# Performance work log

Measured on AMD Instinct MI355X. Metric: run time of the kernel, lower is better.

Reference implementation:

```python
import jax, jax.numpy as jnp
import numpy as np
import math

B, S, D, NH, HFF, E, K, C, L, V = 8, 256, 1024, 16, 2048, 8, 2, 10, 4, 32000
HD = D // NH
EPS = 1e-5


def _pos_encoding(max_len, d_model):
    pos = jnp.arange(max_len, dtype=jnp.float32)[:, None]
    div = jnp.exp(jnp.arange(0, d_model, 2, dtype=jnp.float32) * (-math.log(10000.0) / d_model))
    pe = jnp.zeros((max_len, d_model), dtype=jnp.float32)
    pe = pe.at[:, 0::2].set(jnp.sin(pos * div))
    pe = pe.at[:, 1::2].set(jnp.cos(pos * div))
    return pe[:, None, :]  # [max_len, 1, D], matching torch buffer layout


def _layernorm(x, g, b):
    mu = jnp.mean(x, axis=-1, keepdims=True)
    var = jnp.mean((x - mu) ** 2, axis=-1, keepdims=True)
    return (x - mu) * jax.lax.rsqrt(var + EPS) * g + b


def setup_inputs() -> dict:
    key = jax.random.key(0)
    ks = jax.random.split(key, 20)
    sc = lambda *shape: 0.02
    inp = {
        "src": jax.random.randint(ks[0], (B, S), 0, V, dtype=jnp.int32),
        "emb": jax.random.normal(ks[1], (V, D), jnp.float32) * 0.02,
        "in_proj_w": jax.random.normal(ks[2], (L, 3 * D, D), jnp.float32) * 0.02,
        "in_proj_b": jnp.zeros((L, 3 * D), jnp.float32),
        "out_w": jax.random.normal(ks[3], (L, D, D), jnp.float32) * 0.02,
        "out_b": jnp.zeros((L, D), jnp.float32),
        "ln1_g": jnp.ones((L, D), jnp.float32),
        "ln1_b": jnp.zeros((L, D), jnp.float32),
        "ln2_g": jnp.ones((L, D), jnp.float32),
        "ln2_b": jnp.zeros((L, D), jnp.float32),
        "gate_w": jax.random.normal(ks[4], (L, E, D), jnp.float32) * 0.02,
        "gate_b": jnp.zeros((L, E), jnp.float32),
        "w1": jax.random.normal(ks[5], (L, E, D, HFF), jnp.float32) * 0.02,
        "b1": jnp.zeros((L, E, HFF), jnp.float32),
        "w2": jax.random.normal(ks[6], (L, E, HFF, D), jnp.float32) * 0.02,
        "b2": jnp.zeros((L, E, D), jnp.float32),
        "cls_w": jax.random.normal(ks[7], (C, D), jnp.float32) * 0.02,
        "cls_b": jnp.zeros((C,), jnp.float32),
    }
    return inp


def _attention(x, ipw, ipb, ow, ob):
    # x: [B,S,D]
    qkv = x @ ipw.T + ipb  # [B,S,3D]
    q, k, v = jnp.split(qkv, 3, axis=-1)
    q = q.reshape(B, S, NH, HD)
    k = k.reshape(B, S, NH, HD)
    v = v.reshape(B, S, NH, HD)
    scores = jnp.einsum("bqhd,bkhd->bhqk", q, k) / math.sqrt(HD)
    attn = jax.nn.softmax(scores, axis=-1)
    o = jnp.einsum("bhqk,bkhd->bqhd", attn, v).reshape(B, S, D)
    return o @ ow.T + ob


def _moe(x, gw, gb, w1, b1, w2, b2):
    # x: [B,S,D]; gw: [E,D]; w1: [E,D,H]; w2: [E,H,D]
    t = x.reshape(B * S, D)
    logits = t @ gw.T + gb  # [T,E]
    topv, topi = jax.lax.top_k(logits, K)  # [T,K]
    weights = jax.nn.softmax(topv, axis=-1)  # [T,K]
    # dense expert compute (small E, compute-bound), combine via top-k gather
    h = jax.nn.relu(jnp.einsum("td,edh->teh", t, w1) + b1)  # [T,E,H]
    y = jnp.einsum("teh,ehd->ted", h, w2) + b2  # [T,E,D]
    sel = jnp.take_along_axis(y, topi[:, :, None], axis=1)  # [T,K,D]
    out = jnp.sum(sel * weights[:, :, None], axis=1)  # [T,D]
    return out.reshape(B, S, D), logits.reshape(B, S, E)


def reference(src, emb, in_proj_w, in_proj_b, out_w, out_b, ln1_g, ln1_b,
              ln2_g, ln2_b, gate_w, gate_b, w1, b1, w2, b2, cls_w, cls_b):
    x = emb[src] * math.sqrt(D)  # [B,S,D]
    pe = _pos_encoding(5000, D)  # [max_len,1,D]
    # faithful to original: pe indexed by batch dim (x.size(0)), broadcast over seq
    x = x + pe[:B]  # [B,1,D] -> broadcast [B,S,D]
    all_gates = []
    for l in range(in_proj_w.shape[0]):
        a = _attention(x, in_proj_w[l], in_proj_b[l], out_w[l], out_b[l])
        x = _layernorm(x + a, ln1_g[l], ln1_b[l])
        m, g = _moe(x, gate_w[l], gate_b[l], w1[l], b1[l], w2[l], b2[l])
        x = _layernorm(x + m, ln2_g[l], ln2_b[l])
        all_gates.append(g)
    pooled = jnp.mean(x, axis=1)  # [B,D]
    out = pooled @ cls_w.T + cls_b  # [B,C]
    return out, jnp.stack(all_gates)  # ([B,C], [L,B,S,E])
```

## Files before the change

kernel.cpp:

```cpp
#include <hip/hip_runtime.h>
#include <math.h>

#define TKN 2048
#define DIM 1024
#define NHEAD 16
#define HDIM 64
#define HFF 2048
#define NE 8
#define TOPK 2
#define NCLS 10
#define NLAYER 4
#define SEQ 256
#define BATCH 8

typedef __attribute__((ext_vector_type(8))) _Float16 f16x8;
typedef __attribute__((ext_vector_type(4))) float f32x4;

__device__ __forceinline__ unsigned short f2h(float v) {
  _Float16 h = (_Float16)v;
  return __builtin_bit_cast(unsigned short, h);
}
__device__ __forceinline__ float h2f(unsigned short u) {
  return (float)__builtin_bit_cast(_Float16, u);
}
__device__ __forceinline__ void fsplit(float v, unsigned short& hi, unsigned short& lo) {
  _Float16 h = (_Float16)v;
  hi = __builtin_bit_cast(unsigned short, h);
  lo = f2h(v - (float)h);
}

__device__ __forceinline__ void gload_lds16(const void* g, void* l) {
  __builtin_amdgcn_global_load_lds((__attribute__((address_space(1))) void*)g,
                                   (__attribute__((address_space(3))) void*)l,
                                   16, 0, 0);
}

__global__ __launch_bounds__(256) void k_embed(const int* __restrict__ src,
                                               const float* __restrict__ emb,
                                               float* __restrict__ x,
                                               unsigned short* __restrict__ xhi,
                                               unsigned short* __restrict__ xlo) {
  const int t = blockIdx.x;
  const int tid = threadIdx.x;
  const int b = t / SEQ;
  const int tok = src[t];
  const float* erow = emb + (size_t)tok * DIM;
  const size_t base = (size_t)t * DIM;
  const float cexp = -9.210340371976184f / 1024.0f;
#pragma unroll
  for (int j = 0; j < 4; ++j) {
    int d = tid + 256 * j;
    int i2 = d & ~1;
    float ang = (float)b * expf((float)i2 * cexp);
    float pe = (d & 1) ? cosf(ang) : sinf(ang);
    float v = erow[d] * 32.0f + pe;
    x[base + d] = v;
    fsplit(v, xhi[base + d], xlo[base + d]);
  }
}

__global__ __launch_bounds__(256) void k_cvt_split(const float* __restrict__ in,
                                                   unsigned short* __restrict__ ohi,
                                                   unsigned short* __restrict__ olo) {
  int i = blockIdx.x * 256 + threadIdx.x;
  float4 v = ((const float4*)in)[i];
  ushort4 h, l;
  fsplit(v.x, h.x, l.x); fsplit(v.y, h.y, l.y);
  fsplit(v.z, h.z, l.z); fsplit(v.w, h.w, l.w);
  ((ushort4*)ohi)[i] = h;
  ((ushort4*)olo)[i] = l;
}

__global__ __launch_bounds__(256) void k_cvt_t_split(const float* __restrict__ in,
                                                     unsigned short* __restrict__ ohi,
                                                     unsigned short* __restrict__ olo,
                                                     int R, int Cc) {
  __shared__ float t[32][33];
  const int tx = threadIdx.x & 31, ty = threadIdx.x >> 5;
  const int c0 = blockIdx.x * 32, r0 = blockIdx.y * 32;
  const float* ip = in + (size_t)blockIdx.z * R * Cc;
  const size_t obase = (size_t)blockIdx.z * R * Cc;
#pragma unroll
  for (int j = 0; j < 4; ++j)
    t[ty + 8 * j][tx] = ip[(size_t)(r0 + ty + 8 * j) * Cc + c0 + tx];
  __syncthreads();
#pragma unroll
  for (int j = 0; j < 4; ++j) {
    unsigned short hi, lo;
    fsplit(t[tx][ty + 8 * j], hi, lo);
    size_t o = obase + (size_t)(c0 + ty + 8 * j) * R + r0 + tx;
    ohi[o] = hi;
    olo[o] = lo;
  }
}

template <int MODE, bool RELU, int OUTK, bool SPLIT>
__global__ __launch_bounds__(256) void k_mfma_gemm(
    const unsigned short* __restrict__ Ahi, const unsigned short* __restrict__ Alo,
    const unsigned short* __restrict__ Bhi, const unsigned short* __restrict__ Blo,
    const float* __restrict__ bias, void* __restrict__ out0, void* __restrict__ out1,
    int M, int N, int K,
    const int* __restrict__ slot_token, const int* __restrict__ offg) {
  constexpr int NP = SPLIT ? 2 : 1;
  __shared__ unsigned short As[NP][128][32];
  __shared__ unsigned short Bs[NP][128][32];
  const int tid = threadIdx.x;
  const int w = tid >> 6, lane = tid & 63;
  const int bm = blockIdx.y * 128, bn = blockIdx.x * 128;
  int r0 = 0, rows = M, e = 0;
  if (MODE != 0) {
    e = blockIdx.z;
    r0 = offg[e];
    rows = offg[e + 1] - r0;
    if (bm >= rows) return;
  }
  const size_t bwb = (size_t)e * K * N;
  const float* biasq = bias + (size_t)e * N;

  const int srow = lane >> 2;
  const int skof = (lane & 3) * 8;
  const unsigned short *ah[2], *bh[2], *al[2], *bl[2];
#pragma unroll
  for (int q = 0; q < 2; ++q) {
    int rloc = w * 32 + q * 16 + srow;
    int grow;
    if (MODE == 0) {
      grow = bm + rloc;
    } else {
      int rr = bm + rloc;
      if (rr >= rows) rr = rows - 1;
      grow = (MODE == 1) ? slot_token[r0 + rr] : (r0 + rr);
    }
    size_t ao = (size_t)grow * K + skof;
    size_t bo = bwb + (size_t)(bn + rloc) * K + skof;
    ah[q] = Ahi + ao; bh[q] = Bhi + bo;
    if (SPLIT) { al[q] = Alo + ao; bl[q] = Blo + bo; }
  }

  f32x4 acc[4][4] = {};
  const int wr = w >> 1, wc = w & 1;
  const int lr = lane & 15, lg = lane >> 4;

  for (int k0 = 0; k0 < K; k0 += 32) {
#pragma unroll
    for (int q = 0; q < 2; ++q) {
      const int rb = w * 32 + q * 16;
      gload_lds16(ah[q], &As[0][rb][0]);
      gload_lds16(bh[q], &Bs[0][rb][0]);
      ah[q] += 32; bh[q] += 32;
      if constexpr (SPLIT) {
        gload_lds16(al[q], &As[1][rb][0]);
        gload_lds16(bl[q], &Bs[1][rb][0]);
        al[q] += 32; bl[q] += 32;
      }
    }
    __syncthreads();
    f16x8 afh[4], bfh[4], afl[4], bfl[4];
#pragma unroll
    for (int m = 0; m < 4; ++m)
      afh[m] = *(const f16x8*)&As[0][wr * 64 + m * 16 + lr][lg * 8];
#pragma unroll
    for (int n = 0; n < 4; ++n)
      bfh[n] = *(const f16x8*)&Bs[0][wc * 64 + n * 16 + lr][lg * 8];
    if constexpr (SPLIT) {
#pragma unroll
      for (int m = 0; m < 4; ++m)
        afl[m] = *(const f16x8*)&As[1][wr * 64 + m * 16 + lr][lg * 8];
#pragma unroll
      for (int n = 0; n < 4; ++n)
        bfl[n] = *(const f16x8*)&Bs[1][wc * 64 + n * 16 + lr][lg * 8];
    }
#pragma unroll
    for (int m = 0; m < 4; ++m)
#pragma unroll
      for (int n = 0; n < 4; ++n) {
        acc[m][n] = __builtin_amdgcn_mfma_f32_16x16x32_f16(afh[m], bfh[n], acc[m][n], 0, 0, 0);
        if constexpr (SPLIT) {
          acc[m][n] = __builtin_amdgcn_mfma_f32_16x16x32_f16(afh[m], bfl[n], acc[m][n], 0, 0, 0);
          acc[m][n] = __builtin_amdgcn_mfma_f32_16x16x32_f16(afl[m], bfh[n], acc[m][n], 0, 0, 0);
        }
      }
    __syncthreads();
  }

  float bv[4];
#pragma unroll
  for (int n = 0; n < 4; ++n) bv[n] = biasq[bn + wc * 64 + n * 16 + lr];

#pragma unroll
  for (int m = 0; m < 4; ++m) {
#pragma unroll
    for (int j = 0; j < 4; ++j) {
      int rowg = bm + wr * 64 + m * 16 + lg * 4 + j;
      if (MODE != 0 && rowg >= rows) continue;
      size_t crow = (size_t)((MODE == 0) ? rowg : (r0 + rowg)) * N;
#pragma unroll
      for (int n = 0; n < 4; ++n) {
        float v = acc[m][n][j] + bv[n];
        if (RELU) v = fmaxf(v, 0.f);
        size_t o = crow + bn + wc * 64 + n * 16 + lr;
        if (OUTK == 0) {
          ((float*)out0)[o] = v;
        } else if (OUTK == 1) {
          ((unsigned short*)out0)[o] = f2h(v);
        } else {
          unsigned short hi, lo;
          fsplit(v, hi, lo);
          ((unsigned short*)out0)[o] = hi;
          ((unsigned short*)out1)[o] = lo;
        }
      }
    }
  }
}

__global__ __launch_bounds__(256) void k_attn(const float* __restrict__ qkv,
                                              unsigned short* __restrict__ ohi,
                                              unsigned short* __restrict__ olo) {
  const int qt = blockIdx.x;
  const int hh = blockIdx.y;
  const int bb = blockIdx.z;
  const int tid = threadIdx.x;
  __shared__ float qs[16][64];
  __shared__ float ps[16][256];
  const int t0 = bb * SEQ + qt * 16;
  for (int i = tid; i < 16 * 64; i += 256) {
    int qi = i >> 6, d = i & 63;
    qs[qi][d] = qkv[(size_t)(t0 + qi) * (3 * DIM) + hh * 64 + d];
  }
  __syncthreads();
  float s[16];
#pragma unroll
  for (int qi = 0; qi < 16; ++qi) s[qi] = 0.f;
  const float* krow = qkv + (size_t)(bb * SEQ + tid) * (3 * DIM) + DIM + hh * 64;
#pragma unroll 4
  for (int c = 0; c < 16; ++c) {
    float4 kv = *(const float4*)(krow + c * 4);
#pragma unroll
    for (int qi = 0; qi < 16; ++qi) {
      s[qi] += kv.x * qs[qi][c * 4 + 0] + kv.y * qs[qi][c * 4 + 1] +
               kv.z * qs[qi][c * 4 + 2] + kv.w * qs[qi][c * 4 + 3];
    }
  }
#pragma unroll
  for (int qi = 0; qi < 16; ++qi) ps[qi][tid] = s[qi] * 0.125f;
  __syncthreads();
  const int wv = tid >> 6, lane = tid & 63;
  for (int rr = wv; rr < 16; rr += 4) {
    float v[4];
#pragma unroll
    for (int j = 0; j < 4; ++j) v[j] = ps[rr][lane + 64 * j];
    float m = fmaxf(fmaxf(v[0], v[1]), fmaxf(v[2], v[3]));
    for (int msk = 32; msk; msk >>= 1) m = fmaxf(m, __shfl_xor(m, msk));
    float e[4], sum = 0.f;
#pragma unroll
    for (int j = 0; j < 4; ++j) { e[j] = expf(v[j] - m); sum += e[j]; }
    for (int msk = 32; msk; msk >>= 1) sum += __shfl_xor(sum, msk);
    float inv = 1.0f / sum;
#pragma unroll
    for (int j = 0; j < 4; ++j) ps[rr][lane + 64 * j] = e[j] * inv;
  }
  __syncthreads();
  const int qi0 = tid >> 6, d = tid & 63;
  float acc[4] = {0.f, 0.f, 0.f, 0.f};
  const float* vbase = qkv + (size_t)(bb * SEQ) * (3 * DIM) + 2 * DIM + hh * 64 + d;
  for (int k = 0; k < 256; ++k) {
    float vv = vbase[(size_t)k * (3 * DIM)];
    acc[0] += ps[qi0][k] * vv;
    acc[1] += ps[qi0 + 4][k] * vv;
    acc[2] += ps[qi0 + 8][k] * vv;
    acc[3] += ps[qi0 + 12][k] * vv;
  }
#pragma unroll
  for (int j = 0; j < 4; ++j) {
    size_t o = (size_t)(t0 + qi0 + 4 * j) * DIM + hh * 64 + d;
    fsplit(acc[j], ohi[o], olo[o]);
  }
}

__device__ __forceinline__ float block_reduce_sum(float v, float* red) {
  const int tid = threadIdx.x;
  red[tid] = v;
  __syncthreads();
  for (int s = 128; s > 0; s >>= 1) {
    if (tid < s) red[tid] += red[tid + s];
    __syncthreads();
  }
  float r = red[0];
  __syncthreads();
  return r;
}

__global__ __launch_bounds__(256) void k_add_ln(const float* __restrict__ xin,
                                                const float* __restrict__ add,
                                                const float* __restrict__ g,
                                                const float* __restrict__ bt,
                                                float* __restrict__ xout,
                                                unsigned short* __restrict__ xhi,
                                                unsigned short* __restrict__ xlo) {
  __shared__ float red[256];
  const int t = blockIdx.x, tid = threadIdx.x;
  const size_t base = (size_t)t * DIM;
  float v[4];
  float s = 0.f;
#pragma unroll
  for (int j = 0; j < 4; ++j) {
    int d = tid + 256 * j;
    v[j] = xin[base + d] + add[base + d];
    s += v[j];
  }
  float mean = block_reduce_sum(s, red) * (1.0f / DIM);
  float s2 = 0.f;
#pragma unroll
  for (int j = 0; j < 4; ++j) { float dv = v[j] - mean; s2 += dv * dv; }
  float var = block_reduce_sum(s2, red) * (1.0f / DIM);
  float rs = rsqrtf(var + 1e-5f);
#pragma unroll
  for (int j = 0; j < 4; ++j) {
    int d = tid + 256 * j;
    float o = (v[j] - mean) * rs * g[d] + bt[d];
    xout[base + d] = o;
    fsplit(o, xhi[base + d], xlo[base + d]);
  }
}

__global__ __launch_bounds__(256) void k_gate(const float* __restrict__ x,
                                              const float* __restrict__ gw,
                                              const float* __restrict__ gb,
                                              float* __restrict__ gout,
                                              int* __restrict__ topi,
                                              float* __restrict__ topw) {
  __shared__ float xs[DIM];
  __shared__ float lgs[NE];
  const int t = blockIdx.x, tid = threadIdx.x;
#pragma unroll
  for (int j = 0; j < 4; ++j) xs[tid + 256 * j] = x[(size_t)t * DIM + tid + 256 * j];
  __syncthreads();
  const int eg = tid >> 5, l32 = tid & 31;
  const float* wrow = gw + (size_t)eg * DIM;
  float p = 0.f;
  for (int j = 0; j < 32; ++j) {
    int d = l32 + 32 * j;
    p += xs[d] * wrow[d];
  }
  for (int m = 16; m; m >>= 1) p += __shfl_xor(p, m);
  if (l32 == 0) lgs[eg] = p;
  __syncthreads();
  if (tid < NE) {
    float v = lgs[tid] + gb[tid];
    gout[(size_t)t * NE + tid] = v;
    lgs[tid] = v;
  }
  __syncthreads();
  if (tid == 0) {
    int i0 = 0; float v0 = lgs[0];
    for (int i = 1; i < NE; ++i) if (lgs[i] > v0) { v0 = lgs[i]; i0 = i; }
    int i1 = -1; float v1 = -1e30f;
    for (int i = 0; i < NE; ++i) { if (i == i0) continue; if (lgs[i] > v1) { v1 = lgs[i]; i1 = i; } }
    float e1 = expf(v1 - v0);
    float w0 = 1.0f / (1.0f + e1);
    topi[2 * t] = i0; topi[2 * t + 1] = i1;
    topw[2 * t] = w0; topw[2 * t + 1] = e1 * w0;
  }
}

__global__ __launch_bounds__(512) void k_route(const int* __restrict__ topi,
                                               int* __restrict__ offg,
                                               int* __restrict__ slot_token,
                                               int* __restrict__ slot_of) {
  __shared__ int cnt_s[NE];
  __shared__ int off_s[NE + 1];
  const int tid = threadIdx.x;
  const int w = tid >> 6, lane = tid & 63;
  int c = 0;
  for (int i = lane; i < TKN * TOPK; i += 64) c += (topi[i] == w) ? 1 : 0;
  for (int m = 32; m; m >>= 1) c += __shfl_xor(c, m);
  if (lane == 0) cnt_s[w] = c;
  __syncthreads();
  if (tid == 0) {
    off_s[0] = 0;
    for (int e2 = 0; e2 < NE; ++e2) off_s[e2 + 1] = off_s[e2] + cnt_s[e2];
    for (int e2 = 0; e2 <= NE; ++e2) offg[e2] = off_s[e2];
  }
  __syncthreads();
  int base = off_s[w];
  for (int i0 = 0; i0 < TKN * TOPK; i0 += 64) {
    int i = i0 + lane;
    bool mm = (topi[i] == w);
    unsigned long long mask = __ballot(mm ? 1 : 0);
    int rank = __popcll(mask & ((1ull << lane) - 1ull));
    if (mm) {
      int slot = base + rank;
      slot_token[slot] = i >> 1;
      slot_of[i] = slot;
    }
    base += __popcll(mask);
  }
}

__global__ __launch_bounds__(256) void k_moe_combine_ln(const float* __restrict__ xin,
                                                        const float* __restrict__ y,
                                                        const float* __restrict__ topw,
                                                        const int* __restrict__ slot_of,
                                                        const float* __restrict__ g,
                                                        const float* __restrict__ bt,
                                                        float* __restrict__ xout,
                                                        unsigned short* __restrict__ xhi,
                                                        unsigned short* __restrict__ xlo) {
  __shared__ float red[256];
  const int t = blockIdx.x, tid = threadIdx.x;
  const float w0 = topw[2 * t], w1v = topw[2 * t + 1];
  const int s0 = slot_of[2 * t], s1 = slot_of[2 * t + 1];
  const size_t base = (size_t)t * DIM;
  float v[4];
  float s = 0.f;
#pragma unroll
  for (int j = 0; j < 4; ++j) {
    int d = tid + 256 * j;
    v[j] = xin[base + d] + w0 * y[(size_t)s0 * DIM + d] + w1v * y[(size_t)s1 * DIM + d];
    s += v[j];
  }
  float mean = block_reduce_sum(s, red) * (1.0f / DIM);
  float s2 = 0.f;
#pragma unroll
  for (int j = 0; j < 4; ++j) { float dv = v[j] - mean; s2 += dv * dv; }
  float var = block_reduce_sum(s2, red) * (1.0f / DIM);
  float rs = rsqrtf(var + 1e-5f);
#pragma unroll
  for (int j = 0; j < 4; ++j) {
    int d = tid + 256 * j;
    float o = (v[j] - mean) * rs * g[d] + bt[d];
    xout[base + d] = o;
    fsplit(o, xhi[base + d], xlo[base + d]);
  }
}

__global__ __launch_bounds__(256) void k_pool_cls(const float* __restrict__ x,
                                                  const float* __restrict__ cw,
                                                  const float* __restrict__ cb,
                                                  float* __restrict__ out) {
  __shared__ float pooled[DIM];
  const int b = blockIdx.x, tid = threadIdx.x;
  float a[4] = {0.f, 0.f, 0.f, 0.f};
  for (int s = 0; s < SEQ; ++s) {
    const float* row = x + (size_t)(b * SEQ + s) * DIM;
#pragma unroll
    for (int j = 0; j < 4; ++j) a[j] += row[tid + 256 * j];
  }
#pragma unroll
  for (int j = 0; j < 4; ++j) pooled[tid + 256 * j] = a[j] * (1.0f / SEQ);
  __syncthreads();
  const int wv = tid >> 6, lane = tid & 63;
  for (int c = wv; c < NCLS; c += 4) {
    float p = 0.f;
    for (int d = lane; d < DIM; d += 64) p += pooled[d] * cw[(size_t)c * DIM + d];
    for (int m = 32; m; m >>= 1) p += __shfl_xor(p, m);
    if (lane == 0) out[b * NCLS + c] = p + cb[c];
  }
}

extern "C" void kernel_launch(void* const* d_in, const int* in_sizes, int n_in,
                              void* d_out, int out_size, void* d_ws, size_t ws_size,
                              hipStream_t stream) {
  const int*   src  = (const int*)  d_in[0];
  const float* emb  = (const float*)d_in[1];
  const float* ipw  = (const float*)d_in[2];
  const float* ipb  = (const float*)d_in[3];
  const float* ow   = (const float*)d_in[4];
  const float* ob   = (const float*)d_in[5];
  const float* ln1g = (const float*)d_in[6];
  const float* ln1b = (const float*)d_in[7];
  const float* ln2g = (const float*)d_in[8];
  const float* ln2b = (const float*)d_in[9];
  const float* gw   = (const float*)d_in[10];
  const float* gb   = (const float*)d_in[11];
  const float* w1   = (const float*)d_in[12];
  const float* b1   = (const float*)d_in[13];
  const float* w2   = (const float*)d_in[14];
  const float* b2   = (const float*)d_in[15];
  const float* cw   = (const float*)d_in[16];
  const float* cb   = (const float*)d_in[17];
  float* out = (float*)d_out;

  char* ws = (char*)d_ws;
  size_t off = 0;
  auto carve = [&](size_t bytes) -> void* {
    void* p = ws + off;
    off += (bytes + 255) & ~(size_t)255;
    return p;
  };
  float*          x     = (float*)carve((size_t)TKN * DIM * 4);
  unsigned short* xhi   = (unsigned short*)carve((size_t)TKN * DIM * 2);
  unsigned short* xlo   = (unsigned short*)carve((size_t)TKN * DIM * 2);
  char*           bufQ  = (char*)carve((size_t)2 * TKN * TOPK * HFF * 2);
  float*          qkv   = (float*)bufQ;
  unsigned short* h_hi  = (unsigned short*)bufQ;
  unsigned short* h_lo  = (unsigned short*)(bufQ + (size_t)TKN * TOPK * HFF * 2);
  unsigned short* at_hi = (unsigned short*)carve((size_t)TKN * DIM * 2);
  unsigned short* at_lo = (unsigned short*)carve((size_t)TKN * DIM * 2);
  char*           bufP  = (char*)carve((size_t)TKN * TOPK * DIM * 4);
  float*          proj  = (float*)bufP;
  float*          ybuf  = (float*)bufP;
  unsigned short* wq_hi = (unsigned short*)carve((size_t)3 * DIM * DIM * 2);
  unsigned short* wq_lo = (unsigned short*)carve((size_t)3 * DIM * DIM * 2);
  unsigned short* wo_hi = (unsigned short*)carve((size_t)DIM * DIM * 2);
  unsigned short* wo_lo = (unsigned short*)carve((size_t)DIM * DIM * 2);
  unsigned short* wt_hi = (unsigned short*)carve((size_t)NE * DIM * HFF * 2);
  unsigned short* wt_lo = (unsigned short*)carve((size_t)NE * DIM * HFF * 2);
  float* topw       = (float*)carve((size_t)TKN * TOPK * 4);
  int*   topi       = (int*)  carve((size_t)TKN * TOPK * 4);
  int*   slot_token = (int*)  carve((size_t)TKN * TOPK * 4);
  int*   slot_of    = (int*)  carve((size_t)TKN * TOPK * 4);
  int*   offg       = (int*)  carve(64);

  k_embed<<<TKN, 256, 0, stream>>>(src, emb, x, xhi, xlo);

  for (int l = 0; l < NLAYER; ++l) {
    const float* ipw_l = ipw + (size_t)l * 3 * DIM * DIM;
    const float* ow_l  = ow  + (size_t)l * DIM * DIM;
    const float* w1_l  = w1  + (size_t)l * NE * DIM * HFF;
    const float* w2_l  = w2  + (size_t)l * NE * HFF * DIM;
    const bool sp = (l < NLAYER - 1);

    k_cvt_split<<<(3 * DIM * DIM) / 1024, 256, 0, stream>>>(ipw_l, wq_hi, wq_lo);
    k_cvt_split<<<(DIM * DIM) / 1024, 256, 0, stream>>>(ow_l, wo_hi, wo_lo);
    k_cvt_t_split<<<dim3(HFF / 32, DIM / 32, NE), 256, 0, stream>>>(w1_l, wt_hi, wt_lo, DIM, HFF);

    if (sp)
      k_mfma_gemm<0, false, 0, true><<<dim3(3 * DIM / 128, TKN / 128), 256, 0, stream>>>(
          xhi, xlo, wq_hi, wq_lo, ipb + (size_t)l * 3 * DIM, qkv, nullptr, TKN, 3 * DIM, DIM, nullptr, nullptr);
    else
      k_mfma_gemm<0, false, 0, false><<<dim3(3 * DIM / 128, TKN / 128), 256, 0, stream>>>(
          xhi, xlo, wq_hi, wq_lo, ipb + (size_t)l * 3 * DIM, qkv, nullptr, TKN, 3 * DIM, DIM, nullptr, nullptr);

    k_attn<<<dim3(SEQ / 16, NHEAD, BATCH), 256, 0, stream>>>(qkv, at_hi, at_lo);

    if (sp)
      k_mfma_gemm<0, false, 0, true><<<dim3(DIM / 128, TKN / 128), 256, 0, stream>>>(
          at_hi, at_lo, wo_hi, wo_lo, ob + (size_t)l * DIM, proj, nullptr, TKN, DIM, DIM, nullptr, nullptr);
    else
      k_mfma_gemm<0, false, 0, false><<<dim3(DIM / 128, TKN / 128), 256, 0, stream>>>(
          at_hi, at_lo, wo_hi, wo_lo, ob + (size_t)l * DIM, proj, nullptr, TKN, DIM, DIM, nullptr, nullptr);

    k_add_ln<<<TKN, 256, 0, stream>>>(x, proj, ln1g + l * DIM, ln1b + l * DIM, x, xhi, xlo);

    k_gate<<<TKN, 256, 0, stream>>>(x, gw + (size_t)l * NE * DIM, gb + l * NE,
                                    out + NCLS * BATCH + (size_t)l * TKN * NE, topi, topw);
    k_route<<<1, 512, 0, stream>>>(topi, offg, slot_token, slot_of);

    if (sp)
      k_mfma_gemm<1, true, 2, true><<<dim3(HFF / 128, TKN * TOPK / 128, NE), 256, 0, stream>>>(
          xhi, xlo, wt_hi, wt_lo, b1 + (size_t)l * NE * HFF, h_hi, h_lo, 0, HFF, DIM, slot_token, offg);
    else
      k_mfma_gemm<1, true, 1, false><<<dim3(HFF / 128, TKN * TOPK / 128, NE), 256, 0, stream>>>(
          xhi, xlo, wt_hi, wt_lo, b1 + (size_t)l * NE * HFF, h_hi, nullptr, 0, HFF, DIM, slot_token, offg);

    k_cvt_t_split<<<dim3(DIM / 32, HFF / 32, NE), 256, 0, stream>>>(w2_l, wt_hi, wt_lo, HFF, DIM);

    if (sp)
      k_mfma_gemm<2, false, 0, true><<<dim3(DIM / 128, TKN * TOPK / 128, NE), 256, 0, stream>>>(
          h_hi, h_lo, wt_hi, wt_lo, b2 + (size_t)l * NE * DIM, ybuf, nullptr, 0, DIM, HFF, nullptr, offg);
    else
      k_mfma_gemm<2, false, 0, false><<<dim3(DIM / 128, TKN * TOPK / 128, NE), 256, 0, stream>>>(
          h_hi, h_lo, wt_hi, wt_lo, b2 + (size_t)l * NE * DIM, ybuf, nullptr, 0, DIM, HFF, nullptr, offg);

    k_moe_combine_ln<<<TKN, 256, 0, stream>>>(x, ybuf, topw, slot_of,
                                              ln2g + l * DIM, ln2b + l * DIM, x, xhi, xlo);
  }
  k_pool_cls<<<BATCH, 256, 0, stream>>>(x, cw, cb, out);
}
```

Measured before the change: 1.751 ms.

## Swizzle LDS tile layout to avoid bank conflicts in MFMA GEMM

Stages A and B tiles into one interleaved shared buffer with 64-element rows and an XOR swizzle on 16-byte chunks. Each lane now loads one 8-row slice whose chunk selects hi/lo (or A/B) data. Fragment reads use the matching swizzled offsets. The aim is to remove LDS bank conflicts on the f16x8 fragment reads and reduce load instructions per lane, at the cost of more complex addressing that is easy to get wrong.

New measurement: 1.741 ms. No clear change (-0.6%).

```diff
diff --git a/kernel.cpp b/kernel.cpp
--- a/kernel.cpp
+++ b/kernel.cpp
@@ -101,9 +101,7 @@
     const float* __restrict__ bias, void* __restrict__ out0, void* __restrict__ out1,
     int M, int N, int K,
     const int* __restrict__ slot_token, const int* __restrict__ offg) {
-  constexpr int NP = SPLIT ? 2 : 1;
-  __shared__ unsigned short As[NP][128][32];
-  __shared__ unsigned short Bs[NP][128][32];
+  __shared__ unsigned short U[SPLIT ? 2 : 1][128 * 64];
   const int tid = threadIdx.x;
   const int w = tid >> 6, lane = tid & 63;
   const int bm = blockIdx.y * 128, bn = blockIdx.x * 128;
@@ -117,58 +115,71 @@
   const size_t bwb = (size_t)e * K * N;
   const float* biasq = bias + (size_t)e * N;
 
-  const int srow = lane >> 2;
-  const int skof = (lane & 3) * 8;
-  const unsigned short *ah[2], *bh[2], *al[2], *bl[2];
-#pragma unroll
-  for (int q = 0; q < 2; ++q) {
-    int rloc = w * 32 + q * 16 + srow;
-    int grow;
+  const int lrow8 = lane >> 3;
+  const int s = (lane & 7) ^ lrow8;
+  const int chunk = (s & 3) * 8;
+  const unsigned short* sp0[4];
+  const unsigned short* sp1[4];
+#pragma unroll
+  for (int i = 0; i < 4; ++i) {
+    int rloc = w * 32 + i * 8 + lrow8;
+    int growA;
     if (MODE == 0) {
-      grow = bm + rloc;
+      growA = bm + rloc;
     } else {
       int rr = bm + rloc;
       if (rr >= rows) rr = rows - 1;
-      grow = (MODE == 1) ? slot_token[r0 + rr] : (r0 + rr);
-    }
-    size_t ao = (size_t)grow * K + skof;
-    size_t bo = bwb + (size_t)(bn + rloc) * K + skof;
-    ah[q] = Ahi + ao; bh[q] = Bhi + bo;
-    if (SPLIT) { al[q] = Alo + ao; bl[q] = Blo + bo; }
+      growA = (MODE == 1) ? slot_token[r0 + rr] : (r0 + rr);
+    }
+    size_t aoff = (size_t)growA * K + chunk;
+    size_t boff = bwb + (size_t)(bn + rloc) * K + chunk;
+    if constexpr (SPLIT) {
+      sp0[i] = (s < 4 ? Ahi : Alo) + aoff;
+      sp1[i] = (s < 4 ? Bhi : Blo) + boff;
+    } else {
+      sp0[i] = (s < 4) ? (Ahi + aoff) : (Bhi + boff);
+      sp1[i] = nullptr;
+    }
   }
 
   f32x4 acc[4][4] = {};
   const int wr = w >> 1, wc = w & 1;
   const int lr = lane & 15, lg = lane >> 4;
+  const int sw = lr & 7;
+  unsigned aoffs[4], boffs[4];
+#pragma unroll
+  for (int m = 0; m < 4; ++m)
+    aoffs[m] = (unsigned)((wr * 64 + m * 16 + lr) * 64 + ((lg ^ sw) * 8));
+#pragma unroll
+  for (int n = 0; n < 4; ++n)
+    boffs[n] = (unsigned)((wc * 64 + n * 16 + lr) * 64 + ((lg ^ sw) * 8));
 
   for (int k0 = 0; k0 < K; k0 += 32) {
 #pragma unroll
-    for (int q = 0; q < 2; ++q) {
-      const int rb = w * 32 + q * 16;
-      gload_lds16(ah[q], &As[0][rb][0]);
-      gload_lds16(bh[q], &Bs[0][rb][0]);
-      ah[q] += 32; bh[q] += 32;
+    for (int i = 0; i < 4; ++i) {
+      gload_lds16(sp0[i], &U[0][(w * 32 + i * 8) * 64]);
+      sp0[i] += 32;
       if constexpr (SPLIT) {
-        gload_lds16(al[q], &As[1][rb][0]);
-        gload_lds16(bl[q], &Bs[1][rb][0]);
-        al[q] += 32; bl[q] += 32;
+        gload_lds16(sp1[i], &U[1][(w * 32 + i * 8) * 64]);
+        sp1[i] += 32;
       }
     }
     __syncthreads();
     f16x8 afh[4], bfh[4], afl[4], bfl[4];
-#pragma unroll
-    for (int m = 0; m < 4; ++m)
-      afh[m] = *(const f16x8*)&As[0][wr * 64 + m * 16 + lr][lg * 8];
-#pragma unroll
-    for (int n = 0; n < 4; ++n)
-      bfh[n] = *(const f16x8*)&Bs[0][wc * 64 + n * 16 + lr][lg * 8];
     if constexpr (SPLIT) {
 #pragma unroll
-      for (int m = 0; m < 4; ++m)
-        afl[m] = *(const f16x8*)&As[1][wr * 64 + m * 16 + lr][lg * 8];
-#pragma unroll
-      for (int n = 0; n < 4; ++n)
-        bfl[n] = *(const f16x8*)&Bs[1][wc * 64 + n * 16 + lr][lg * 8];
+      for (int m = 0; m < 4; ++m) afh[m] = *(const f16x8*)&U[0][aoffs[m]];
+#pragma unroll
+      for (int m = 0; m < 4; ++m) afl[m] = *(const f16x8*)&U[0][aoffs[m] ^ 32];
+#pragma unroll
+      for (int n = 0; n < 4; ++n) bfh[n] = *(const f16x8*)&U[1][boffs[n]];
+#pragma unroll
+      for (int n = 0; n < 4; ++n) bfl[n] = *(const f16x8*)&U[1][boffs[n] ^ 32];
+    } else {
+#pragma unroll
+      for (int m = 0; m < 4; ++m) afh[m] = *(const f16x8*)&U[0][aoffs[m]];
+#pragma unroll
+      for (int n = 0; n < 4; ++n) bfh[n] = *(const f16x8*)&U[0][boffs[n] ^ 32];
     }
 #pragma unroll
     for (int m = 0; m < 4; ++m)
```
